# Optimization experiments

Measured on AMD Instinct MI355X. Metric: run time of the kernel, lower is better.

## Reference

```python
import jax, jax.numpy as jnp
import numpy as np

B, S1, S2, D1, D2, F = 8, 2048, 2048, 512, 512, 256

def setup_inputs() -> dict:
    key = jax.random.key(0)
    ks = jax.random.split(key, 10)
    sc1 = 1.0 / np.sqrt(D1)
    sc2 = 1.0 / np.sqrt(D2)
    scf = 1.0 / np.sqrt(F)
    return {
        "feat1": jax.random.normal(ks[0], (B, S1, D1), jnp.float32),
        "feat2": jax.random.normal(ks[1], (B, S2, D2), jnp.float32),
        "Wq": jax.random.normal(ks[2], (D1, F), jnp.float32) * sc1,
        "bq": jnp.zeros((F,), jnp.float32),
        "Wk": jax.random.normal(ks[3], (D2, F), jnp.float32) * sc2,
        "bk": jnp.zeros((F,), jnp.float32),
        "Wv": jax.random.normal(ks[4], (D2, F), jnp.float32) * sc2,
        "bv": jnp.zeros((F,), jnp.float32),
        "Wfc": jax.random.normal(ks[5], (F, F), jnp.float32) * scf,
        "bfc": jnp.zeros((F,), jnp.float32),
    }

def reference(feat1, feat2, Wq, bq, Wk, bk, Wv, bv, Wfc, bfc):
    Q = jnp.einsum('bsd,df->bsf', feat1, Wq) + bq          # [B,S1,F]
    K = jnp.einsum('btd,df->btf', feat2, Wk) + bk          # [B,S2,F]
    V = jnp.einsum('btd,df->btf', feat2, Wv) + bv          # [B,S2,F]
    scores = jnp.einsum('bsf,btf->bst', Q, K) / jnp.sqrt(jnp.float32(K.shape[-1]))
    attn = jax.nn.softmax(scores, axis=-1)                 # [B,S1,S2]
    attn_out = jnp.einsum('bst,btf->bsf', attn, V)         # [B,S1,F]
    out = jnp.einsum('bsf,fg->bsg', attn_out, Wfc) + bfc   # [B,S1,F]
    return out
```

## Files before the change

kernel.cpp:

```cpp
#include <hip/hip_runtime.h>
#include <hip/hip_bf16.h>

#define B_ 8
#define S1_ 2048
#define S2_ 2048
#define D_ 512
#define F_ 256

typedef __attribute__((ext_vector_type(4))) float f32x4;
typedef __attribute__((ext_vector_type(8))) short s16x8;
typedef __attribute__((ext_vector_type(4))) short s16x4;

__device__ __forceinline__ short f2bf(float x) {
  union { float f; unsigned u; } v; v.f = x;
  unsigned r = v.u + 0x7fffu + ((v.u >> 16) & 1u);
  return (short)(r >> 16);
}

__device__ __forceinline__ int pk2bf(float a, float b) {
  union { __hip_bfloat162 h; int i; } u;
  u.h = __float22bfloat162_rn(make_float2(a, b));
  return u.i;
}

__global__ __launch_bounds__(256) void wtrans_kernel(
    const float* __restrict__ Wq, const float* __restrict__ Wk,
    const float* __restrict__ Wv, const float* __restrict__ Wfc,
    short* __restrict__ Wqt, short* __restrict__ Wkt,
    short* __restrict__ Wvt, short* __restrict__ Wfct) {
  int y = blockIdx.y;
  const float* W; short* Wt; int D;
  if (y == 0)      { W = Wq;  Wt = Wqt;  D = 512; }
  else if (y == 1) { W = Wk;  Wt = Wkt;  D = 512; }
  else if (y == 2) { W = Wv;  Wt = Wvt;  D = 512; }
  else             { W = Wfc; Wt = Wfct; D = 256; }
  int tiles_d = D >> 6;
  int bx = blockIdx.x;
  if (bx >= tiles_d * 4) return;
  int d0 = (bx % tiles_d) * 64, f0 = (bx / tiles_d) * 64;

  __shared__ short Ts[64][68];
  int t = threadIdx.x;
  int r = t >> 2, c16 = (t & 3) * 16;
  {
    const float* src = W + (size_t)(d0 + r) * F_ + f0 + c16;
    f32x4 v0 = *(const f32x4*)(src);
    f32x4 v1 = *(const f32x4*)(src + 4);
    f32x4 v2 = *(const f32x4*)(src + 8);
    f32x4 v3 = *(const f32x4*)(src + 12);
    s16x8 s0, s1;
    ((int*)&s0)[0] = pk2bf(v0[0], v0[1]); ((int*)&s0)[1] = pk2bf(v0[2], v0[3]);
    ((int*)&s0)[2] = pk2bf(v1[0], v1[1]); ((int*)&s0)[3] = pk2bf(v1[2], v1[3]);
    ((int*)&s1)[0] = pk2bf(v2[0], v2[1]); ((int*)&s1)[1] = pk2bf(v2[2], v2[3]);
    ((int*)&s1)[2] = pk2bf(v3[0], v3[1]); ((int*)&s1)[3] = pk2bf(v3[2], v3[3]);
    *(s16x8*)(&Ts[r][c16]) = s0;
    *(s16x8*)(&Ts[r][c16 + 8]) = s1;
  }
  __syncthreads();
  {
    int fr = t >> 2, dc16 = (t & 3) * 16;
    s16x8 o0, o1;
    for (int j = 0; j < 8; ++j) o0[j] = Ts[dc16 + j][fr];
    for (int j = 0; j < 8; ++j) o1[j] = Ts[dc16 + 8 + j][fr];
    short* dst = Wt + (size_t)(f0 + fr) * D + d0 + dc16;
    *(s16x8*)dst = o0;
    *(s16x8*)(dst + 8) = o1;
  }
}

__global__ __launch_bounds__(256, 3) void proj_kernel(
    const float* __restrict__ feat1, const float* __restrict__ feat2,
    const short* __restrict__ Wqt, const short* __restrict__ Wkt,
    const short* __restrict__ Wvt,
    const float* __restrict__ bq, const float* __restrict__ bk,
    const float* __restrict__ bv,
    short* __restrict__ Qw, short* __restrict__ Kw, short* __restrict__ Vtw) {
  const float* A; const short* Wt; const float* bias; short* outp;
  float scale; int trans;
  if (blockIdx.y == 0)      { A = feat1; Wt = Wqt; bias = bq; outp = Qw;  scale = 0.0625f; trans = 0; }
  else if (blockIdx.y == 1) { A = feat2; Wt = Wkt; bias = bk; outp = Kw;  scale = 1.0f;    trans = 0; }
  else                      { A = feat2; Wt = Wvt; bias = bv; outp = Vtw; scale = 1.0f;    trans = 1; }

  __shared__ __align__(16) short As[64][72];
  __shared__ __align__(16) short Ws[256][72];

  int m0 = blockIdx.x * 64;
  int t = threadIdx.x;
  int w = t >> 6, L = t & 63, rowA = L & 15, quad = L >> 4;
  int ar = t >> 2, ac16 = (t & 3) * 16;

  f32x4 acc[4][4];
  for (int i = 0; i < 4; ++i)
    for (int j = 0; j < 4; ++j) acc[i][j] = (f32x4){0.f, 0.f, 0.f, 0.f};

  for (int k0 = 0; k0 < D_; k0 += 64) {
    {
      const float* src = A + (size_t)(m0 + ar) * D_ + k0 + ac16;
      f32x4 v0 = *(const f32x4*)(src);
      f32x4 v1 = *(const f32x4*)(src + 4);
      f32x4 v2 = *(const f32x4*)(src + 8);
      f32x4 v3 = *(const f32x4*)(src + 12);
      s16x8 s0, s1;
      ((int*)&s0)[0] = pk2bf(v0[0], v0[1]); ((int*)&s0)[1] = pk2bf(v0[2], v0[3]);
      ((int*)&s0)[2] = pk2bf(v1[0], v1[1]); ((int*)&s0)[3] = pk2bf(v1[2], v1[3]);
      ((int*)&s1)[0] = pk2bf(v2[0], v2[1]); ((int*)&s1)[1] = pk2bf(v2[2], v2[3]);
      ((int*)&s1)[2] = pk2bf(v3[0], v3[1]); ((int*)&s1)[3] = pk2bf(v3[2], v3[3]);
      *(s16x8*)(&As[ar][ac16]) = s0;
      *(s16x8*)(&As[ar][ac16 + 8]) = s1;
    }
    for (int p = 0; p < 4; ++p) {
      int r = (t >> 2) + p * 64;
      const short* src = Wt + (size_t)r * D_ + k0 + ac16;
      *(s16x8*)(&Ws[r][ac16]) = *(const s16x8*)(src);
      *(s16x8*)(&Ws[r][ac16 + 8]) = *(const s16x8*)(src + 8);
    }
    __syncthreads();
    for (int kt = 0; kt < 2; ++kt) {
      s16x8 a[4];
      for (int mt = 0; mt < 4; ++mt)
        a[mt] = *(const s16x8*)(&As[mt * 16 + rowA][kt * 32 + quad * 8]);
      for (int nt = 0; nt < 4; ++nt) {
        s16x8 bfr = *(const s16x8*)(&Ws[w * 64 + nt * 16 + rowA][kt * 32 + quad * 8]);
        for (int mt = 0; mt < 4; ++mt)
          acc[mt][nt] = __builtin_amdgcn_mfma_f32_16x16x32_bf16(a[mt], bfr, acc[mt][nt], 0, 0, 0);
      }
    }
    __syncthreads();
  }

  if (!trans) {
    float bn[4];
    for (int nt = 0; nt < 4; ++nt) bn[nt] = bias[w * 64 + nt * 16 + rowA];
    for (int mt = 0; mt < 4; ++mt) {
      int m = m0 + mt * 16 + quad * 4;
      for (int nt = 0; nt < 4; ++nt) {
        int n = w * 64 + nt * 16 + rowA;
        for (int r = 0; r < 4; ++r)
          outp[(size_t)(m + r) * F_ + n] = f2bf((acc[mt][nt][r] + bn[nt]) * scale);
      }
    }
  } else {
    int bb = m0 >> 11;
    int tbase = m0 & (S2_ - 1);
    float bn[4];
    for (int nt = 0; nt < 4; ++nt) bn[nt] = bias[w * 64 + nt * 16 + rowA];
    for (int nt = 0; nt < 4; ++nt) {
      int f = w * 64 + nt * 16 + rowA;
      for (int mt = 0; mt < 4; ++mt) {
        int tt = tbase + mt * 16 + quad * 4;
        s16x4 o;
        for (int r = 0; r < 4; ++r) o[r] = f2bf(acc[mt][nt][r] + bn[nt]);
        *(s16x4*)(outp + ((size_t)bb * F_ + f) * S2_ + tt) = o;
      }
    }
  }
}

__global__ __launch_bounds__(512, 2) void flash_kernel(
    const short* __restrict__ Q,
    const short* __restrict__ K,
    const short* __restrict__ Vt,
    short* __restrict__ O) {
  __shared__ __align__(16) short Ks[2][64][264];
  __shared__ __align__(16) short Vs[2][256][72];
  __shared__ __align__(16) short Ps[2][64][72];

  int b = blockIdx.x & 7;
  int s0 = (blockIdx.x >> 3) * 64;
  int t = threadIdx.x;
  int w = t >> 6, L = t & 63, rowA = L & 15, quad = L >> 4;
  int isS = (w < 4);

  const short* Kb = K + (size_t)b * S2_ * F_;
  const short* Vb = Vt + (size_t)b * F_ * S2_;

  int kr = t >> 5, kc8 = (t & 31) * 8;
  int vr = t >> 3, vc8 = (t & 7) * 8;

  int rs = (w & 1) * 32, cs = ((w >> 1) & 1) * 32;
  int mg = (w - 4) & 1, fg = ((w - 4) >> 1) & 1;

  s16x8 qf[2][8];
  if (isS) {
    const short* Qb = Q + ((size_t)b * S1_ + s0 + rs) * F_;
    for (int mt = 0; mt < 2; ++mt)
      for (int kt = 0; kt < 8; ++kt)
        qf[mt][kt] = *(const s16x8*)(Qb + (size_t)(mt * 16 + rowA) * F_ + kt * 32 + quad * 8);
  }
  f32x4 o[2][8];
  for (int i = 0; i < 2; ++i)
    for (int j = 0; j < 8; ++j) o[i][j] = (f32x4){0.f, 0.f, 0.f, 0.f};
  float l_lane[2] = {0.f, 0.f};

  s16x8 kpre[4], vpre[4];
  for (int p = 0; p < 4; ++p)
    kpre[p] = *(const s16x8*)(Kb + (size_t)(kr + p * 16) * F_ + kc8);
  for (int p = 0; p < 4; ++p)
    *(s16x8*)(&Ks[0][kr + p * 16][kc8]) = kpre[p];
  for (int p = 0; p < 4; ++p)
    kpre[p] = *(const s16x8*)(Kb + (size_t)(64 + kr + p * 16) * F_ + kc8);
  for (int p = 0; p < 4; ++p)
    vpre[p] = *(const s16x8*)(Vb + (size_t)(vr + p * 64) * S2_ + vc8);

  for (int it = 0; it <= 32; ++it) {
    int cb = it & 1;
    __syncthreads();
    if (it < 32) {
      for (int p = 0; p < 4; ++p)
        *(s16x8*)(&Vs[cb][vr + p * 64][vc8]) = vpre[p];
      if (it < 31) {
        for (int p = 0; p < 4; ++p)
          *(s16x8*)(&Ks[1 - cb][kr + p * 16][kc8]) = kpre[p];
        int n0 = (it + 1) * 64;
        for (int p = 0; p < 4; ++p)
          vpre[p] = *(const s16x8*)(Vb + (size_t)(vr + p * 64) * S2_ + n0 + vc8);
      }
      if (it < 30) {
        int n0 = (it + 2) * 64;
        for (int p = 0; p < 4; ++p)
          kpre[p] = *(const s16x8*)(Kb + (size_t)(n0 + kr + p * 16) * F_ + kc8);
      }
    }
    if (isS) {
      if (it < 32) {
        f32x4 s[2][2];
        for (int i = 0; i < 2; ++i)
          for (int j = 0; j < 2; ++j) s[i][j] = (f32x4){0.f, 0.f, 0.f, 0.f};
        for (int kt = 0; kt < 8; ++kt) {
          s16x8 bf0 = *(const s16x8*)(&Ks[cb][cs + rowA][kt * 32 + quad * 8]);
          s16x8 bf1 = *(const s16x8*)(&Ks[cb][cs + 16 + rowA][kt * 32 + quad * 8]);
          for (int mt = 0; mt < 2; ++mt) {
            s[mt][0] = __builtin_amdgcn_mfma_f32_16x16x32_bf16(bf0, qf[mt][kt], s[mt][0], 0, 0, 0);
            s[mt][1] = __builtin_amdgcn_mfma_f32_16x16x32_bf16(bf1, qf[mt][kt], s[mt][1], 0, 0, 0);
          }
        }
        for (int mt = 0; mt < 2; ++mt)
          for (int j = 0; j < 2; ++j) {
            s16x4 pk;
            for (int r = 0; r < 4; ++r) {
              float p = __expf(s[mt][j][r]);
              l_lane[mt] += p;
              pk[r] = f2bf(p);
            }
            *(s16x4*)(&Ps[cb][rs + mt * 16 + rowA][cs + j * 16 + quad * 4]) = pk;
          }
      }
    } else {
      if (it > 0) {
        int pb = 1 - cb;
        s16x8 pa[2][2];
        for (int mt = 0; mt < 2; ++mt)
          for (int kt = 0; kt < 2; ++kt)
            pa[mt][kt] = *(const s16x8*)(&Ps[pb][mg * 32 + mt * 16 + rowA][kt * 32 + quad * 8]);
        for (int ft = 0; ft < 8; ++ft)
          for (int kt = 0; kt < 2; ++kt) {
            s16x8 vf = *(const s16x8*)(&Vs[pb][fg * 128 + ft * 16 + rowA][kt * 32 + quad * 8]);
            for (int mt = 0; mt < 2; ++mt)
              o[mt][ft] = __builtin_amdgcn_mfma_f32_16x16x32_bf16(pa[mt][kt], vf, o[mt][ft], 0, 0, 0);
          }
      }
    }
  }

  float* lf = (float*)&Ks[0][0][0];
  if (isS) {
    for (int mt = 0; mt < 2; ++mt) {
      float x = l_lane[mt];
      x += __shfl_xor(x, 16, 64);
      x += __shfl_xor(x, 32, 64);
      if (L < 16)
        lf[((w >> 1) & 1) * 64 + rs + mt * 16 + rowA] = x;
    }
  }
  __syncthreads();
  if (!isS) {
    short* Ob = O + ((size_t)b * S1_ + s0) * F_;
    for (int mt = 0; mt < 2; ++mt)
      for (int r = 0; r < 4; ++r) {
        int row = mg * 32 + mt * 16 + quad * 4 + r;
        float inv = 1.0f / (lf[row] + lf[64 + row]);
        for (int ft = 0; ft < 8; ++ft)
          Ob[(size_t)row * F_ + fg * 128 + ft * 16 + rowA] = f2bf(o[mt][ft][r] * inv);
      }
  }
}

__global__ __launch_bounds__(256) void fc_kernel(
    const short* __restrict__ AO,
    const short* __restrict__ Wt,
    const float* __restrict__ bias,
    float* __restrict__ out) {
  __shared__ __align__(16) short As[64][72];
  __shared__ __align__(16) short Ws[128][72];

  int m0 = blockIdx.x * 64;
  int n0 = blockIdx.y * 128;
  int t = threadIdx.x;
  int w = t >> 6, L = t & 63, rowA = L & 15, quad = L >> 4;
  int wy = w & 1, wx = w >> 1;

  int ar = t >> 2, ac16 = (t & 3) * 16;
  int wr = t >> 1, wc32 = (t & 1) * 32;

  s16x8 apre[2], wpre[4];
  {
    const short* asrc = AO + (size_t)(m0 + ar) * F_ + ac16;
    apre[0] = *(const s16x8*)(asrc);
    apre[1] = *(const s16x8*)(asrc + 8);
    const short* wsrc = Wt + (size_t)(n0 + wr) * F_ + wc32;
    for (int j = 0; j < 4; ++j) wpre[j] = *(const s16x8*)(wsrc + j * 8);
  }

  f32x4 acc[2][4];
  for (int i = 0; i < 2; ++i)
    for (int j = 0; j < 4; ++j) acc[i][j] = (f32x4){0.f, 0.f, 0.f, 0.f};

  for (int k0 = 0; k0 < F_; k0 += 64) {
    *(s16x8*)(&As[ar][ac16]) = apre[0];
    *(s16x8*)(&As[ar][ac16 + 8]) = apre[1];
    for (int j = 0; j < 4; ++j) *(s16x8*)(&Ws[wr][wc32 + j * 8]) = wpre[j];
    __syncthreads();
    if (k0 + 64 < F_) {
      const short* asrc = AO + (size_t)(m0 + ar) * F_ + k0 + 64 + ac16;
      apre[0] = *(const s16x8*)(asrc);
      apre[1] = *(const s16x8*)(asrc + 8);
      const short* wsrc = Wt + (size_t)(n0 + wr) * F_ + k0 + 64 + wc32;
      for (int j = 0; j < 4; ++j) wpre[j] = *(const s16x8*)(wsrc + j * 8);
    }
    for (int kt = 0; kt < 2; ++kt) {
      s16x8 a[2];
      for (int mt = 0; mt < 2; ++mt)
        a[mt] = *(const s16x8*)(&As[wy * 32 + mt * 16 + rowA][kt * 32 + quad * 8]);
      for (int nt = 0; nt < 4; ++nt) {
        s16x8 bfr = *(const s16x8*)(&Ws[wx * 64 + nt * 16 + rowA][kt * 32 + quad * 8]);
        for (int mt = 0; mt < 2; ++mt)
          acc[mt][nt] = __builtin_amdgcn_mfma_f32_16x16x32_bf16(a[mt], bfr, acc[mt][nt], 0, 0, 0);
      }
    }
    __syncthreads();
  }

  float bn[4];
  for (int nt = 0; nt < 4; ++nt) bn[nt] = bias[n0 + wx * 64 + nt * 16 + rowA];
  for (int mt = 0; mt < 2; ++mt) {
    int m = m0 + wy * 32 + mt * 16 + quad * 4;
    for (int nt = 0; nt < 4; ++nt) {
      int n = n0 + wx * 64 + nt * 16 + rowA;
      for (int r = 0; r < 4; ++r)
        out[(size_t)(m + r) * F_ + n] = acc[mt][nt][r] + bn[nt];
    }
  }
}

extern "C" void kernel_launch(void* const* d_in, const int* in_sizes, int n_in,
                              void* d_out, int out_size, void* d_ws, size_t ws_size,
                              hipStream_t stream) {
  const float* feat1 = (const float*)d_in[0];
  const float* feat2 = (const float*)d_in[1];
  const float* Wq  = (const float*)d_in[2];
  const float* bq  = (const float*)d_in[3];
  const float* Wk  = (const float*)d_in[4];
  const float* bk  = (const float*)d_in[5];
  const float* Wv  = (const float*)d_in[6];
  const float* bv  = (const float*)d_in[7];
  const float* Wfc = (const float*)d_in[8];
  const float* bfc = (const float*)d_in[9];
  float* out = (float*)d_out;
  char* ws = (char*)d_ws;

  short* Qw   = (short*)(ws);
  short* Kw   = (short*)(ws + (size_t)(8u  << 20));
  short* Vtw  = (short*)(ws + (size_t)(16u << 20));
  short* AOw  = (short*)(ws + (size_t)(24u << 20));
  short* Wqt  = (short*)(ws + (size_t)(32u << 20));
  short* Wkt  = Wqt + 256 * 512;
  short* Wvt  = Wkt + 256 * 512;
  short* Wfct = Wvt + 256 * 512;

  wtrans_kernel<<<dim3(32, 4), 256, 0, stream>>>(Wq, Wk, Wv, Wfc, Wqt, Wkt, Wvt, Wfct);
  proj_kernel<<<dim3(256, 3), 256, 0, stream>>>(feat1, feat2, Wqt, Wkt, Wvt,
                                                bq, bk, bv, Qw, Kw, Vtw);
  flash_kernel<<<dim3(256), 512, 0, stream>>>(Qw, Kw, Vtw, AOw);
  fc_kernel<<<dim3(256, 2), 256, 0, stream>>>(AOw, Wfct, bfc, out);
}
```

Before: 183.4 us.

## Load V fragments directly from global into registers, drop LDS staging

The PV warps now fetch their V operand fragments directly from global memory into registers, prefetching the next tile after each MFMA pass, instead of staging V through a double-buffered shared-memory tile. This removes the large Vs LDS buffer and its store/load traffic and frees shared memory. In exchange, warps sharing an F half load duplicate data, the global accesses are less coalesced, and the kernel uses more registers for the prefetch buffer, with less latency hiding.

```diff
diff --git a/kernel.cpp b/kernel.cpp
--- a/kernel.cpp
+++ b/kernel.cpp
@@ -162,7 +162,6 @@
     const short* __restrict__ Vt,
     short* __restrict__ O) {
   __shared__ __align__(16) short Ks[2][64][264];
-  __shared__ __align__(16) short Vs[2][256][72];
   __shared__ __align__(16) short Ps[2][64][72];
 
   int b = blockIdx.x & 7;
@@ -175,7 +174,6 @@
   const short* Vb = Vt + (size_t)b * F_ * S2_;
 
   int kr = t >> 5, kc8 = (t & 31) * 8;
-  int vr = t >> 3, vc8 = (t & 7) * 8;
 
   int rs = (w & 1) * 32, cs = ((w >> 1) & 1) * 32;
   int mg = (w - 4) & 1, fg = ((w - 4) >> 1) & 1;
@@ -192,29 +190,30 @@
     for (int j = 0; j < 8; ++j) o[i][j] = (f32x4){0.f, 0.f, 0.f, 0.f};
   float l_lane[2] = {0.f, 0.f};
 
-  s16x8 kpre[4], vpre[4];
+  s16x8 kpre[4];
   for (int p = 0; p < 4; ++p)
     kpre[p] = *(const s16x8*)(Kb + (size_t)(kr + p * 16) * F_ + kc8);
   for (int p = 0; p < 4; ++p)
     *(s16x8*)(&Ks[0][kr + p * 16][kc8]) = kpre[p];
   for (int p = 0; p < 4; ++p)
     kpre[p] = *(const s16x8*)(Kb + (size_t)(64 + kr + p * 16) * F_ + kc8);
-  for (int p = 0; p < 4; ++p)
-    vpre[p] = *(const s16x8*)(Vb + (size_t)(vr + p * 64) * S2_ + vc8);
+
+  const short* Vw = Vb + (size_t)(fg * 128 + rowA) * S2_ + quad * 8;
+  s16x8 vfp[8][2];
+  if (!isS) {
+#pragma unroll
+    for (int ft = 0; ft < 8; ++ft)
+#pragma unroll
+      for (int kt = 0; kt < 2; ++kt)
+        vfp[ft][kt] = *(const s16x8*)(Vw + (size_t)(ft * 16) * S2_ + kt * 32);
+  }
 
   for (int it = 0; it <= 32; ++it) {
     int cb = it & 1;
     __syncthreads();
-    if (it < 32) {
+    if (it < 31) {
       for (int p = 0; p < 4; ++p)
-        *(s16x8*)(&Vs[cb][vr + p * 64][vc8]) = vpre[p];
-      if (it < 31) {
-        for (int p = 0; p < 4; ++p)
-          *(s16x8*)(&Ks[1 - cb][kr + p * 16][kc8]) = kpre[p];
-        int n0 = (it + 1) * 64;
-        for (int p = 0; p < 4; ++p)
-          vpre[p] = *(const s16x8*)(Vb + (size_t)(vr + p * 64) * S2_ + n0 + vc8);
-      }
+        *(s16x8*)(&Ks[1 - cb][kr + p * 16][kc8]) = kpre[p];
       if (it < 30) {
         int n0 = (it + 2) * 64;
         for (int p = 0; p < 4; ++p)
@@ -252,12 +251,20 @@
         for (int mt = 0; mt < 2; ++mt)
           for (int kt = 0; kt < 2; ++kt)
             pa[mt][kt] = *(const s16x8*)(&Ps[pb][mg * 32 + mt * 16 + rowA][kt * 32 + quad * 8]);
+#pragma unroll
         for (int ft = 0; ft < 8; ++ft)
-          for (int kt = 0; kt < 2; ++kt) {
-            s16x8 vf = *(const s16x8*)(&Vs[pb][fg * 128 + ft * 16 + rowA][kt * 32 + quad * 8]);
+#pragma unroll
+          for (int kt = 0; kt < 2; ++kt)
             for (int mt = 0; mt < 2; ++mt)
-              o[mt][ft] = __builtin_amdgcn_mfma_f32_16x16x32_bf16(pa[mt][kt], vf, o[mt][ft], 0, 0, 0);
-          }
+              o[mt][ft] = __builtin_amdgcn_mfma_f32_16x16x32_bf16(pa[mt][kt], vfp[ft][kt], o[mt][ft], 0, 0, 0);
+        if (it < 32) {
+          int n0 = it * 64;
+#pragma unroll
+          for (int ft = 0; ft < 8; ++ft)
+#pragma unroll
+            for (int kt = 0; kt < 2; ++kt)
+              vfp[ft][kt] = *(const s16x8*)(Vw + (size_t)(ft * 16) * S2_ + n0 + kt * 32);
+        }
       }
     }
   }
```

New measurement: 207.7 us. 13.2% more time.

## Fuse K and V projections into shared blocks reading feat2 once

Applied to the files above, without the earlier changes.

The projection kernel now uses a 1D grid: the first 256 blocks compute Q as before, and the remaining 512 blocks each take 32 rows of feat2 and compute both K and V from one bf16-converted A tile, using a K-step of 32. This halves global reads and fp32-to-bf16 conversion of feat2, which were previously done separately for K and V. The cost is smaller per-block M tiles, more weight-tile traffic per output row (both Wk and Wv loaded for every 32 rows), and more syncs per block.

```diff
diff --git a/kernel.cpp b/kernel.cpp
--- a/kernel.cpp
+++ b/kernel.cpp
@@ -75,82 +75,135 @@
     const float* __restrict__ bq, const float* __restrict__ bk,
     const float* __restrict__ bv,
     short* __restrict__ Qw, short* __restrict__ Kw, short* __restrict__ Vtw) {
-  const float* A; const short* Wt; const float* bias; short* outp;
-  float scale; int trans;
-  if (blockIdx.y == 0)      { A = feat1; Wt = Wqt; bias = bq; outp = Qw;  scale = 0.0625f; trans = 0; }
-  else if (blockIdx.y == 1) { A = feat2; Wt = Wkt; bias = bk; outp = Kw;  scale = 1.0f;    trans = 0; }
-  else                      { A = feat2; Wt = Wvt; bias = bv; outp = Vtw; scale = 1.0f;    trans = 1; }
-
-  __shared__ __align__(16) short As[64][72];
-  __shared__ __align__(16) short Ws[256][72];
-
-  int m0 = blockIdx.x * 64;
+  __shared__ __align__(16) char smem[46080];
+
   int t = threadIdx.x;
   int w = t >> 6, L = t & 63, rowA = L & 15, quad = L >> 4;
-  int ar = t >> 2, ac16 = (t & 3) * 16;
-
-  f32x4 acc[4][4];
-  for (int i = 0; i < 4; ++i)
-    for (int j = 0; j < 4; ++j) acc[i][j] = (f32x4){0.f, 0.f, 0.f, 0.f};
-
-  for (int k0 = 0; k0 < D_; k0 += 64) {
-    {
-      const float* src = A + (size_t)(m0 + ar) * D_ + k0 + ac16;
-      f32x4 v0 = *(const f32x4*)(src);
-      f32x4 v1 = *(const f32x4*)(src + 4);
-      f32x4 v2 = *(const f32x4*)(src + 8);
-      f32x4 v3 = *(const f32x4*)(src + 12);
-      s16x8 s0, s1;
-      ((int*)&s0)[0] = pk2bf(v0[0], v0[1]); ((int*)&s0)[1] = pk2bf(v0[2], v0[3]);
-      ((int*)&s0)[2] = pk2bf(v1[0], v1[1]); ((int*)&s0)[3] = pk2bf(v1[2], v1[3]);
-      ((int*)&s1)[0] = pk2bf(v2[0], v2[1]); ((int*)&s1)[1] = pk2bf(v2[2], v2[3]);
-      ((int*)&s1)[2] = pk2bf(v3[0], v3[1]); ((int*)&s1)[3] = pk2bf(v3[2], v3[3]);
-      *(s16x8*)(&As[ar][ac16]) = s0;
-      *(s16x8*)(&As[ar][ac16 + 8]) = s1;
-    }
-    for (int p = 0; p < 4; ++p) {
-      int r = (t >> 2) + p * 64;
-      const short* src = Wt + (size_t)r * D_ + k0 + ac16;
-      *(s16x8*)(&Ws[r][ac16]) = *(const s16x8*)(src);
-      *(s16x8*)(&Ws[r][ac16 + 8]) = *(const s16x8*)(src + 8);
-    }
-    __syncthreads();
-    for (int kt = 0; kt < 2; ++kt) {
-      s16x8 a[4];
-      for (int mt = 0; mt < 4; ++mt)
-        a[mt] = *(const s16x8*)(&As[mt * 16 + rowA][kt * 32 + quad * 8]);
-      for (int nt = 0; nt < 4; ++nt) {
-        s16x8 bfr = *(const s16x8*)(&Ws[w * 64 + nt * 16 + rowA][kt * 32 + quad * 8]);
+
+  if (blockIdx.x < 256) {
+    short (*As)[72] = (short (*)[72])smem;
+    short (*Ws)[72] = (short (*)[72])(smem + 9216);
+    int m0 = blockIdx.x * 64;
+    int ar = t >> 2, ac16 = (t & 3) * 16;
+
+    f32x4 acc[4][4];
+    for (int i = 0; i < 4; ++i)
+      for (int j = 0; j < 4; ++j) acc[i][j] = (f32x4){0.f, 0.f, 0.f, 0.f};
+
+    for (int k0 = 0; k0 < D_; k0 += 64) {
+      {
+        const float* src = feat1 + (size_t)(m0 + ar) * D_ + k0 + ac16;
+        f32x4 v0 = *(const f32x4*)(src);
+        f32x4 v1 = *(const f32x4*)(src + 4);
+        f32x4 v2 = *(const f32x4*)(src + 8);
+        f32x4 v3 = *(const f32x4*)(src + 12);
+        s16x8 s0, s1;
+        ((int*)&s0)[0] = pk2bf(v0[0], v0[1]); ((int*)&s0)[1] = pk2bf(v0[2], v0[3]);
+        ((int*)&s0)[2] = pk2bf(v1[0], v1[1]); ((int*)&s0)[3] = pk2bf(v1[2], v1[3]);
+        ((int*)&s1)[0] = pk2bf(v2[0], v2[1]); ((int*)&s1)[1] = pk2bf(v2[2], v2[3]);
+        ((int*)&s1)[2] = pk2bf(v3[0], v3[1]); ((int*)&s1)[3] = pk2bf(v3[2], v3[3]);
+        *(s16x8*)(&As[ar][ac16]) = s0;
+        *(s16x8*)(&As[ar][ac16 + 8]) = s1;
+      }
+      for (int p = 0; p < 4; ++p) {
+        int r = (t >> 2) + p * 64;
+        const short* src = Wqt + (size_t)r * D_ + k0 + ac16;
+        *(s16x8*)(&Ws[r][ac16]) = *(const s16x8*)(src);
+        *(s16x8*)(&Ws[r][ac16 + 8]) = *(const s16x8*)(src + 8);
+      }
+      __syncthreads();
+      for (int kt = 0; kt < 2; ++kt) {
+        s16x8 a[4];
         for (int mt = 0; mt < 4; ++mt)
-          acc[mt][nt] = __builtin_amdgcn_mfma_f32_16x16x32_bf16(a[mt], bfr, acc[mt][nt], 0, 0, 0);
-      }
-    }
-    __syncthreads();
-  }
-
-  if (!trans) {
+          a[mt] = *(const s16x8*)(&As[mt * 16 + rowA][kt * 32 + quad * 8]);
+        for (int nt = 0; nt < 4; ++nt) {
+          s16x8 bfr = *(const s16x8*)(&Ws[w * 64 + nt * 16 + rowA][kt * 32 + quad * 8]);
+          for (int mt = 0; mt < 4; ++mt)
+            acc[mt][nt] = __builtin_amdgcn_mfma_f32_16x16x32_bf16(a[mt], bfr, acc[mt][nt], 0, 0, 0);
+        }
+      }
+      __syncthreads();
+    }
+
     float bn[4];
-    for (int nt = 0; nt < 4; ++nt) bn[nt] = bias[w * 64 + nt * 16 + rowA];
+    for (int nt = 0; nt < 4; ++nt) bn[nt] = bq[w * 64 + nt * 16 + rowA];
     for (int mt = 0; mt < 4; ++mt) {
       int m = m0 + mt * 16 + quad * 4;
       for (int nt = 0; nt < 4; ++nt) {
         int n = w * 64 + nt * 16 + rowA;
         for (int r = 0; r < 4; ++r)
-          outp[(size_t)(m + r) * F_ + n] = f2bf((acc[mt][nt][r] + bn[nt]) * scale);
+          Qw[(size_t)(m + r) * F_ + n] = f2bf((acc[mt][nt][r] + bn[nt]) * 0.0625f);
       }
     }
   } else {
+    short (*As32)[40] = (short (*)[40])smem;
+    short (*Wks)[40]  = (short (*)[40])(smem + 2560);
+    short (*Wvs)[40]  = (short (*)[40])(smem + 2560 + 20480);
+    int m0 = (blockIdx.x - 256) * 32;
+    int ar = t >> 3, ac4 = (t & 7) * 4;
+    int wr = t >> 1, wc16 = (t & 1) * 16;
+
+    f32x4 acck[2][4], accv[2][4];
+    for (int i = 0; i < 2; ++i)
+      for (int j = 0; j < 4; ++j) {
+        acck[i][j] = (f32x4){0.f, 0.f, 0.f, 0.f};
+        accv[i][j] = (f32x4){0.f, 0.f, 0.f, 0.f};
+      }
+
+    for (int k0 = 0; k0 < D_; k0 += 32) {
+      {
+        f32x4 v0 = *(const f32x4*)(feat2 + (size_t)(m0 + ar) * D_ + k0 + ac4);
+        s16x4 s;
+        ((int*)&s)[0] = pk2bf(v0[0], v0[1]);
+        ((int*)&s)[1] = pk2bf(v0[2], v0[3]);
+        *(s16x4*)(&As32[ar][ac4]) = s;
+      }
+      for (int p = 0; p < 2; ++p) {
+        int r = wr + p * 128;
+        const short* srck = Wkt + (size_t)r * D_ + k0 + wc16;
+        *(s16x8*)(&Wks[r][wc16])     = *(const s16x8*)(srck);
+        *(s16x8*)(&Wks[r][wc16 + 8]) = *(const s16x8*)(srck + 8);
+        const short* srcv = Wvt + (size_t)r * D_ + k0 + wc16;
+        *(s16x8*)(&Wvs[r][wc16])     = *(const s16x8*)(srcv);
+        *(s16x8*)(&Wvs[r][wc16 + 8]) = *(const s16x8*)(srcv + 8);
+      }
+      __syncthreads();
+      s16x8 a[2];
+      for (int mt = 0; mt < 2; ++mt)
+        a[mt] = *(const s16x8*)(&As32[mt * 16 + rowA][quad * 8]);
+      for (int nt = 0; nt < 4; ++nt) {
+        s16x8 bk_ = *(const s16x8*)(&Wks[w * 64 + nt * 16 + rowA][quad * 8]);
+        for (int mt = 0; mt < 2; ++mt)
+          acck[mt][nt] = __builtin_amdgcn_mfma_f32_16x16x32_bf16(a[mt], bk_, acck[mt][nt], 0, 0, 0);
+        s16x8 bv_ = *(const s16x8*)(&Wvs[w * 64 + nt * 16 + rowA][quad * 8]);
+        for (int mt = 0; mt < 2; ++mt)
+          accv[mt][nt] = __builtin_amdgcn_mfma_f32_16x16x32_bf16(a[mt], bv_, accv[mt][nt], 0, 0, 0);
+      }
+      __syncthreads();
+    }
+
+    float bnk[4], bnv[4];
+    for (int nt = 0; nt < 4; ++nt) {
+      bnk[nt] = bk[w * 64 + nt * 16 + rowA];
+      bnv[nt] = bv[w * 64 + nt * 16 + rowA];
+    }
+    for (int mt = 0; mt < 2; ++mt) {
+      int m = m0 + mt * 16 + quad * 4;
+      for (int nt = 0; nt < 4; ++nt) {
+        int n = w * 64 + nt * 16 + rowA;
+        for (int r = 0; r < 4; ++r)
+          Kw[(size_t)(m + r) * F_ + n] = f2bf(acck[mt][nt][r] + bnk[nt]);
+      }
+    }
     int bb = m0 >> 11;
     int tbase = m0 & (S2_ - 1);
-    float bn[4];
-    for (int nt = 0; nt < 4; ++nt) bn[nt] = bias[w * 64 + nt * 16 + rowA];
     for (int nt = 0; nt < 4; ++nt) {
       int f = w * 64 + nt * 16 + rowA;
-      for (int mt = 0; mt < 4; ++mt) {
+      for (int mt = 0; mt < 2; ++mt) {
         int tt = tbase + mt * 16 + quad * 4;
         s16x4 o;
-        for (int r = 0; r < 4; ++r) o[r] = f2bf(acc[mt][nt][r] + bn[nt]);
-        *(s16x4*)(outp + ((size_t)bb * F_ + f) * S2_ + tt) = o;
+        for (int r = 0; r < 4; ++r) o[r] = f2bf(accv[mt][nt][r] + bnv[nt]);
+        *(s16x4*)(Vtw + ((size_t)bb * F_ + f) * S2_ + tt) = o;
       }
     }
   }
@@ -378,8 +431,8 @@
   short* Wfct = Wvt + 256 * 512;
 
   wtrans_kernel<<<dim3(32, 4), 256, 0, stream>>>(Wq, Wk, Wv, Wfc, Wqt, Wkt, Wvt, Wfct);
-  proj_kernel<<<dim3(256, 3), 256, 0, stream>>>(feat1, feat2, Wqt, Wkt, Wvt,
-                                                bq, bk, bv, Qw, Kw, Vtw);
+  proj_kernel<<<dim3(768), 256, 0, stream>>>(feat1, feat2, Wqt, Wkt, Wvt,
+                                             bq, bk, bv, Qw, Kw, Vtw);
   flash_kernel<<<dim3(256), 512, 0, stream>>>(Qw, Kw, Vtw, AOw);
   fc_kernel<<<dim3(256, 2), 256, 0, stream>>>(AOw, Wfct, bfc, out);
 }
```

After: 203.9 us. +11.1%, slower.
